# Kernel tuning notes

Measured on AMD Instinct MI355X. Metric: run time of the kernel, lower is better.

## Reference

```python
import jax, jax.numpy as jnp
import numpy as np

B, T, D, V, L = 128, 1024, 512, 128, 128
BLANK = V - 1          # keras ctc_batch_cost uses num_classes-1 as blank
EPS = 1e-7             # tf.keras.backend.epsilon()
NEG = jnp.float32(-1e30)


def setup_inputs() -> dict:
    key = jax.random.key(0)
    k1, k2, k3, k4 = jax.random.split(key, 4)
    x = jax.random.normal(k1, (B, T, D), jnp.float32)
    W = jax.random.normal(k2, (D, V), jnp.float32) / np.sqrt(D)
    b = jnp.zeros((V,), jnp.float32)
    targets = jax.random.randint(k3, (B, L), 0, V - 1, dtype=jnp.int32)   # labels in [0, V-2]
    targets_length = jax.random.randint(k4, (B,), 16, L + 1, dtype=jnp.int32)  # >=1
    return {"x": x, "W": W, "b": b, "targets": targets, "targets_length": targets_length}


def _ctc_neg_log_lik(log_probs, targets, targets_length):
    # log_probs: [B,T,V]; targets: [B,L]; returns per-example -log p(targets | probs)
    Bb, Tt, Vv = log_probs.shape
    Ll = targets.shape[1]
    S = 2 * Ll + 1
    # extended label sequence: blank, l1, blank, l2, ..., blank   [B,S]
    ext = jnp.full((Bb, S), BLANK, dtype=targets.dtype)
    ext = ext.at[:, 1::2].set(targets)
    # allow skip transition s-2 -> s when ext[s] != blank and ext[s] != ext[s-2]
    ext2 = jnp.concatenate([jnp.full((Bb, 2), -1, ext.dtype), ext[:, :-2]], axis=1)
    allow2 = (ext != BLANK) & (ext != ext2)                       # [B,S]

    def emit(logp_t):  # logp_t [B,V] -> [B,S]
        return jnp.take_along_axis(logp_t, ext, axis=1)

    # t = 0: only s=0 (blank) and s=1 (first label) reachable
    e0 = emit(log_probs[:, 0])
    alpha0 = jnp.where(jnp.arange(S)[None, :] < 2, e0, NEG)       # [B,S]

    def step(alpha, logp_t):
        a1 = jnp.concatenate([jnp.full((Bb, 1), NEG), alpha[:, :-1]], axis=1)
        a2 = jnp.concatenate([jnp.full((Bb, 2), NEG), alpha[:, :-2]], axis=1)
        m = jnp.logaddexp(alpha, a1)
        m = jnp.where(allow2, jnp.logaddexp(m, a2), m)
        return m + emit(logp_t), None

    alpha_T, _ = jax.lax.scan(step, alpha0, jnp.swapaxes(log_probs, 0, 1)[1:])
    # final states: s = 2*len (trailing blank) and s = 2*len - 1 (last label)
    last = 2 * targets_length                                     # [B]
    aN = jnp.take_along_axis(alpha_T, last[:, None], axis=1)[:, 0]
    aN1 = jnp.take_along_axis(alpha_T, (last - 1)[:, None], axis=1)[:, 0]
    return -jnp.logaddexp(aN, aN1)                                # [B]


def reference(x, W, b, targets, targets_length):
    # Dense -> Softmax (module outputs probabilities) -> ctc_batch_cost: log(p + eps) -> CTC DP -> sum
    probs = jax.nn.softmax(jnp.einsum("btd,dv->btv", x, W) + b, axis=-1)
    log_probs = jnp.log(probs + EPS)
    loss = _ctc_neg_log_lik(log_probs, targets, targets_length)
    return jnp.sum(loss)
```

## Files before the change

kernel.cpp:

```cpp
#include <hip/hip_runtime.h>

#define Bb 128
#define Tt 1024
#define Dd 512
#define Vv 128
#define Ll 128
#define EPSF 1e-7f
#define PADK 72
#define NEGF -1e30f

typedef float f4 __attribute__((ext_vector_type(4)));
typedef short s8 __attribute__((ext_vector_type(8)));
typedef float f32x4 __attribute__((ext_vector_type(4)));

__device__ inline unsigned int f2bf(float f) {
    unsigned int u = __float_as_uint(f);
    return (u + 0x7fffu + ((u >> 16) & 1u)) >> 16;
}

__device__ inline float lae2(float x, float y) {
    float m = fmaxf(x, y);
    float d = fminf(x, y) - m;
    return m + __logf(1.f + __expf(d));
}

__device__ inline float dpp_shr1(float v) {
    return __int_as_float(__builtin_amdgcn_update_dpp(
        0, __float_as_int(v), 0x138, 0xf, 0xf, false));
}
__device__ inline int dpp_shr1_i(int v) {
    return __builtin_amdgcn_update_dpp(0, v, 0x138, 0xf, 0xf, false);
}

__global__ void wt_kernel(const float* __restrict__ W, unsigned short* __restrict__ Wt) {
    int idx = blockIdx.x * 256 + threadIdx.x;
    int v = idx >> 9, k = idx & 511;
    Wt[idx] = (unsigned short)f2bf(W[k * Vv + v]);
}

__global__ __launch_bounds__(256) void gemm_softmax(
    const float* __restrict__ x, const unsigned short* __restrict__ Wt,
    const float* __restrict__ bias, float* __restrict__ LP)
{
    __shared__ float lds[128 * 128];
    __shared__ __align__(16) float invs[128];
    unsigned short* Al = (unsigned short*)lds;
    unsigned short* Bl = Al + 128 * PADK;

    const int tid = threadIdx.x;
    const int wave = tid >> 6, lane = tid & 63;
    const int lm = lane & 15, lq = lane >> 4;
    const int wm = (wave >> 1) << 6, wn = (wave & 1) << 6;
    const long row0 = (long)blockIdx.x << 7;

    f32x4 acc[4][4];
    #pragma unroll
    for (int i = 0; i < 4; i++)
        #pragma unroll
        for (int j = 0; j < 4; j++)
            acc[i][j] = (f32x4){0.f, 0.f, 0.f, 0.f};

    for (int k0 = 0; k0 < Dd; k0 += 64) {
        __syncthreads();
        #pragma unroll
        for (int i = 0; i < 8; i++) {
            int idx = tid + (i << 8);
            int r = idx >> 4, c4 = idx & 15;
            f4 v = *(const f4*)(x + (row0 + r) * Dd + k0 + (c4 << 2));
            unsigned long long q =
                (unsigned long long)(f2bf(v.x) | (f2bf(v.y) << 16)) |
                ((unsigned long long)(f2bf(v.z) | (f2bf(v.w) << 16)) << 32);
            *(unsigned long long*)(Al + r * PADK + (c4 << 2)) = q;
        }
        #pragma unroll
        for (int i = 0; i < 4; i++) {
            int idx = tid + (i << 8);
            int vr = idx >> 3, c = idx & 7;
            f4 w = *(const f4*)(Wt + vr * 512 + k0 + (c << 3));
            *(f4*)(Bl + vr * PADK + (c << 3)) = w;
        }
        __syncthreads();
        #pragma unroll
        for (int kk = 0; kk < 64; kk += 32) {
            s8 af[4], bfr[4];
            #pragma unroll
            for (int mi = 0; mi < 4; mi++)
                af[mi] = *(const s8*)(Al + (wm + (mi << 4) + lm) * PADK + kk + (lq << 3));
            #pragma unroll
            for (int ni = 0; ni < 4; ni++)
                bfr[ni] = *(const s8*)(Bl + (wn + (ni << 4) + lm) * PADK + kk + (lq << 3));
            #pragma unroll
            for (int mi = 0; mi < 4; mi++)
                #pragma unroll
                for (int ni = 0; ni < 4; ni++)
                    acc[mi][ni] = __builtin_amdgcn_mfma_f32_16x16x32_bf16(
                        af[mi], bfr[ni], acc[mi][ni], 0, 0, 0);
        }
    }
    __syncthreads();
    #pragma unroll
    for (int mi = 0; mi < 4; mi++) {
        #pragma unroll
        for (int ni = 0; ni < 4; ni++) {
            int col = wn + (ni << 4) + lm;
            float bv = bias[col];
            #pragma unroll
            for (int r = 0; r < 4; r++) {
                int row = wm + (mi << 4) + (lq << 2) + r;
                int word = (row << 7) + ((((col >> 2) ^ ((row >> 2) & 7)) & 31) << 2) + (col & 3);
                lds[word] = acc[mi][ni][r] + bv;
            }
        }
    }
    __syncthreads();
    if (tid < 128) {
        int row = tid;
        float m = -1e30f;
        #pragma unroll
        for (int cc = 0; cc < 32; cc++) {
            int word = (row << 7) + (((cc + row) & 31) << 2);
            f4 v = *(const f4*)(lds + word);
            m = fmaxf(m, fmaxf(fmaxf(v.x, v.y), fmaxf(v.z, v.w)));
        }
        float s = 0.f;
        #pragma unroll
        for (int cc = 0; cc < 32; cc++) {
            int word = (row << 7) + (((cc + row) & 31) << 2);
            f4 v = *(f4*)(lds + word);
            v.x = __expf(v.x - m); v.y = __expf(v.y - m);
            v.z = __expf(v.z - m); v.w = __expf(v.w - m);
            s += v.x + v.y + v.z + v.w;
            *(f4*)(lds + word) = v;
        }
        invs[row] = 1.f / s;
    }
    __syncthreads();
    {
        const int l = tid & 31, g = tid >> 5;
        const int bidx = blockIdx.x >> 3;
        const int tbase = (blockIdx.x & 7) << 7;
        const f4 iv = *(const f4*)(invs + (l << 2));
        #pragma unroll
        for (int jj = 0; jj < 16; jj++) {
            const int v = (g << 4) + jj;
            const int swz = ((v >> 2) ^ (l & 7)) << 2;
            const int r0 = v & 3;
            f4 o;
            #pragma unroll
            for (int r = 0; r < 4; r++) {
                int t = (l << 2) + r;
                o[r] = fmaf(lds[(t << 7) + swz + r0], iv[r], EPSF);
            }
            *(f4*)(LP + ((long)bidx * Vv + v) * Tt + tbase + (l << 2)) = o;
        }
    }
}

__global__ __launch_bounds__(64) void ctc_kernel(
    const float* __restrict__ PT, const int* __restrict__ targets,
    const int* __restrict__ tlen, float* __restrict__ out)
{
    const int b = blockIdx.x;
    const int lane = threadIdx.x;
    const float* baseP = PT + (long)b * Vv * Tt;

    const int tgt0 = targets[(b << 7) + (lane << 1)];
    const int tgt1 = targets[(b << 7) + (lane << 1) + 1];
    int tp = __shfl_up(tgt1, 1);
    if (lane == 0) tp = -1;
    const bool mA = (tgt0 != tp);
    const bool mB = (tgt1 != tgt0);
    const float mBf = mB ? 1.f : 0.f;

    const float* pB = baseP + 127 * Tt;
    const float* p0 = baseP + (long)tgt0 * Tt;
    const float* p1 = baseP + (long)tgt1 * Tt;

    float u0 = (lane == 0) ? pB[0] : 0.f;
    float u1 = (lane == 0) ? p0[0] : 0.f;
    float u2 = 0.f, u3 = 0.f, u4 = 0.f;
    int anc = 0;
    float fprev = 1.f;
    float fprevA = mA ? 1.f : 0.f;

    f4 Xb[4], Xs[4], Xt[4], Yb[4], Ys[4], Yt[4], Zb[4], Zs[4], Zt[4];

#define LOADW(BUF, W) do {                                                  \
    int tn_ = ((W) < 63 ? (W) : 63) << 4;                                   \
    _Pragma("unroll")                                                       \
    for (int q = 0; q < 4; q++) {                                           \
        BUF##b[q] = *(const f4*)(pB + tn_ + (q << 2));                      \
        BUF##s[q] = *(const f4*)(p0 + tn_ + (q << 2));                      \
        BUF##t[q] = *(const f4*)(p1 + tn_ + (q << 2));                      \
    } } while (0)

#define DOSTEP(BUF, i) do {                                                 \
    float lb = BUF##b[(i) >> 2][(i) & 3];                                   \
    float l0 = BUF##s[(i) >> 2][(i) & 3];                                   \
    float l1 = BUF##t[(i) >> 2][(i) & 3];                                   \
    float s_ = dpp_shr1(u3);                                \
    float t01 = u0 + u1;                                                    \
    float n0 = fmaf(s_, fprev,  u0) * lb;                                   \
    float n1 = fmaf(s_, fprevA, t01) * l0;                                  \
    float n2 = (u1 + u2) * lb;                                              \
    float n3 = fmaf(u1, mBf, u2 + u3) * l1;                                 \
    float n4 = (u3 + u4) * lb;                                              \
    u0 = n0; u1 = n1; u2 = n2; u3 = n3; u4 = n4; } while (0)

#define RESCALE(ADOPT) do {                                                 \
    float umax = fmaxf(fmaxf(fmaxf(u0, u1), fmaxf(u2, u3)), u4);            \
    int e = (int)((__float_as_uint(umax) >> 23) & 0xffu) - 126;             \
    float sc = __uint_as_float((unsigned)(127 - e) << 23);        \
    u0 *= sc; u1 *= sc; u2 *= sc; u3 *= sc; u4 *= sc;       \
    if (ADOPT) {                                                            \
        bool live = umax > 0.f;                                             \
        anc = live ? (anc + e) : anc;                                       \
        _Pragma("unroll")                                                   \
        for (int r_ = 0; r_ < 3; r_++) {                                    \
            int cp_ = dpp_shr1_i(anc);                                      \
            anc = live ? anc : cp_;                                         \
        }                                                                   \
    } else {                                                                \
        anc += e;                                                           \
    }                                                                       \
    int cp = dpp_shr1_i(anc);                                               \
    int d_ = cp - anc;                                                      \
    d_ = d_ > 96 ? 96 : d_;                     \
    fprev = (d_ < -126) ? 0.f                                               \
           : __uint_as_float((unsigned)((d_ + 127) << 23));                 \
    fprevA = mA ? fprev : 0.f; } while (0)

#define WINDOW(CUR, N2, W, ADOPT, ISTART) do {                              \
    LOADW(N2, (W) + 2);                                                     \
    _Pragma("unroll")                                                       \
    for (int i = ISTART; i < 16; i++) {                                     \
        DOSTEP(CUR, i);                                                     \
        if ((i & 3) == 3) RESCALE(ADOPT);                                   \
    } } while (0)

    LOADW(X, 0);
    LOADW(Y, 1);
    WINDOW(X, Z, 0, true, 1);
    for (int g = 0; g < 5; g++) {
        int w = 1 + 3 * g;
        WINDOW(Y, X, w,     true, 0);
        WINDOW(Z, Y, w + 1, true, 0);
        WINDOW(X, Z, w + 2, true, 0);
    }
    for (int g = 0; g < 16; g++) {
        int w = 16 + 3 * g;
        WINDOW(Y, X, w,     false, 0);
        WINDOW(Z, Y, w + 1, false, 0);
        WINDOW(X, Z, w + 2, false, 0);
    }

    __shared__ float af[257];
    const float LN2 = 0.69314718056f;
    float fa = (float)anc;
    af[(lane << 2) + 0] = u0 > 0.f ? (fa + log2f(u0)) * LN2 : NEGF;
    af[(lane << 2) + 1] = u1 > 0.f ? (fa + log2f(u1)) * LN2 : NEGF;
    af[(lane << 2) + 2] = u2 > 0.f ? (fa + log2f(u2)) * LN2 : NEGF;
    af[(lane << 2) + 3] = u3 > 0.f ? (fa + log2f(u3)) * LN2 : NEGF;
    if (lane == 63) af[256] = u4 > 0.f ? (fa + log2f(u4)) * LN2 : NEGF;
    __syncthreads();
    if (lane == 0) {
        int len = tlen[b];
        float loss = -lae2(af[2 * len], af[2 * len - 1]);
        atomicAdd(out, loss);
    }
}

extern "C" void kernel_launch(void* const* d_in, const int* in_sizes, int n_in,
                              void* d_out, int out_size, void* d_ws, size_t ws_size,
                              hipStream_t stream) {
    const float* x       = (const float*)d_in[0];
    const float* W       = (const float*)d_in[1];
    const float* bias    = (const float*)d_in[2];
    const int*   targets = (const int*)d_in[3];
    const int*   tl      = (const int*)d_in[4];
    float* out = (float*)d_out;

    float* LP = (float*)d_ws;
    unsigned short* Wt = (unsigned short*)((char*)d_ws + (size_t)Bb * Tt * Vv * 4);

    (void)hipMemsetAsync(out, 0, sizeof(float), stream);
    wt_kernel<<<256, 256, 0, stream>>>(W, Wt);
    gemm_softmax<<<1024, 256, 0, stream>>>(x, Wt, bias, LP);
    ctc_kernel<<<Bb, 64, 0, stream>>>(LP, targets, tl, out);
}
```

Before: 434.1 us.

## Double-buffer GEMM LDS tiles with register prefetch and split softmax rows

The GEMM K-loop now prefetches the next x/W tile into registers while MFMAs run on the current LDS buffer, using two ping-pong LDS buffers so only one barrier is needed per tile. The fp32-to-bf16 conversion uses the hardware v_cvt_pk_bf16_f32 instruction instead of manual integer rounding. Softmax row reductions are split across all 256 threads (two per row, combined with shuffles) instead of 128. The aim is to hide global load latency and shorten the epilogue, at the cost of more LDS (72KB) and more registers, which may lower occupancy.

```diff
diff --git a/kernel.cpp b/kernel.cpp
--- a/kernel.cpp
+++ b/kernel.cpp
@@ -42,10 +42,13 @@
     const float* __restrict__ x, const unsigned short* __restrict__ Wt,
     const float* __restrict__ bias, float* __restrict__ LP)
 {
-    __shared__ float lds[128 * 128];
+    __shared__ __align__(16) char smem[73728];
     __shared__ __align__(16) float invs[128];
-    unsigned short* Al = (unsigned short*)lds;
-    unsigned short* Bl = Al + 128 * PADK;
+    unsigned short* Al0 = (unsigned short*)smem;
+    unsigned short* Al1 = (unsigned short*)(smem + 18432);
+    unsigned short* Bl0 = (unsigned short*)(smem + 36864);
+    unsigned short* Bl1 = (unsigned short*)(smem + 55296);
+    float* lds = (float*)smem;
 
     const int tid = threadIdx.x;
     const int wave = tid >> 6, lane = tid & 63;
@@ -60,41 +63,78 @@
         for (int j = 0; j < 4; j++)
             acc[i][j] = (f32x4){0.f, 0.f, 0.f, 0.f};
 
-    for (int k0 = 0; k0 < Dd; k0 += 64) {
+    f4 ra[8], rb[4];
+
+#define STAGE_REGS(K0) do {                                                 \
+    int kb_ = (K0) << 6;                                                    \
+    _Pragma("unroll")                                                       \
+    for (int i = 0; i < 8; i++) {                                           \
+        int idx = tid + (i << 8);                                           \
+        int r = idx >> 4, c4 = idx & 15;                                    \
+        ra[i] = *(const f4*)(x + (row0 + r) * Dd + kb_ + (c4 << 2));        \
+    }                                                                       \
+    _Pragma("unroll")                                                       \
+    for (int i = 0; i < 4; i++) {                                           \
+        int idx = tid + (i << 8);                                           \
+        int vr = idx >> 3, c = idx & 7;                                     \
+        rb[i] = *(const f4*)(Wt + vr * 512 + kb_ + (c << 3));               \
+    } } while (0)
+
+#define WRITE_LDS(AL, BL) do {                                              \
+    _Pragma("unroll")                                                       \
+    for (int i = 0; i < 8; i++) {                                           \
+        int idx = tid + (i << 8);                                           \
+        int r = idx >> 4, c4 = idx & 15;                                    \
+        unsigned int lo_, hi_;                                              \
+        asm("v_cvt_pk_bf16_f32 %0, %1, %2" : "=v"(lo_)                      \
+            : "v"(ra[i].x), "v"(ra[i].y));                                  \
+        asm("v_cvt_pk_bf16_f32 %0, %1, %2" : "=v"(hi_)                      \
+            : "v"(ra[i].z), "v"(ra[i].w));                                  \
+        unsigned long long q_ = (unsigned long long)lo_                     \
+                              | ((unsigned long long)hi_ << 32);            \
+        *(unsigned long long*)((AL) + r * PADK + (c4 << 2)) = q_;           \
+    }                                                                       \
+    _Pragma("unroll")                                                       \
+    for (int i = 0; i < 4; i++) {                                           \
+        int idx = tid + (i << 8);                                           \
+        int vr = idx >> 3, c = idx & 7;                                     \
+        *(f4*)((BL) + vr * PADK + (c << 3)) = rb[i];                        \
+    } } while (0)
+
+#define MFMA_TILE(AL, BL) do {                                              \
+    _Pragma("unroll")                                                       \
+    for (int kk = 0; kk < 64; kk += 32) {                                   \
+        s8 afr[4], bfr[4];                                                  \
+        _Pragma("unroll")                                                   \
+        for (int mi = 0; mi < 4; mi++)                                      \
+            afr[mi] = *(const s8*)((AL) + (wm + (mi << 4) + lm) * PADK      \
+                                    + kk + (lq << 3));                      \
+        _Pragma("unroll")                                                   \
+        for (int ni = 0; ni < 4; ni++)                                      \
+            bfr[ni] = *(const s8*)((BL) + (wn + (ni << 4) + lm) * PADK      \
+                                    + kk + (lq << 3));                      \
+        _Pragma("unroll")                                                   \
+        for (int mi = 0; mi < 4; mi++)                                      \
+            _Pragma("unroll")                                               \
+            for (int ni = 0; ni < 4; ni++)                                  \
+                acc[mi][ni] = __builtin_amdgcn_mfma_f32_16x16x32_bf16(      \
+                    afr[mi], bfr[ni], acc[mi][ni], 0, 0, 0);                \
+    } } while (0)
+
+    STAGE_REGS(0);
+    WRITE_LDS(Al0, Bl0);
+    __syncthreads();
+    #pragma unroll
+    for (int s = 0; s < 4; s++) {
+        STAGE_REGS(2 * s + 1);
+        MFMA_TILE(Al0, Bl0);
+        WRITE_LDS(Al1, Bl1);
         __syncthreads();
-        #pragma unroll
-        for (int i = 0; i < 8; i++) {
-            int idx = tid + (i << 8);
-            int r = idx >> 4, c4 = idx & 15;
-            f4 v = *(const f4*)(x + (row0 + r) * Dd + k0 + (c4 << 2));
-            unsigned long long q =
-                (unsigned long long)(f2bf(v.x) | (f2bf(v.y) << 16)) |
-                ((unsigned long long)(f2bf(v.z) | (f2bf(v.w) << 16)) << 32);
-            *(unsigned long long*)(Al + r * PADK + (c4 << 2)) = q;
-        }
-        #pragma unroll
-        for (int i = 0; i < 4; i++) {
-            int idx = tid + (i << 8);
-            int vr = idx >> 3, c = idx & 7;
-            f4 w = *(const f4*)(Wt + vr * 512 + k0 + (c << 3));
-            *(f4*)(Bl + vr * PADK + (c << 3)) = w;
-        }
-        __syncthreads();
-        #pragma unroll
-        for (int kk = 0; kk < 64; kk += 32) {
-            s8 af[4], bfr[4];
-            #pragma unroll
-            for (int mi = 0; mi < 4; mi++)
-                af[mi] = *(const s8*)(Al + (wm + (mi << 4) + lm) * PADK + kk + (lq << 3));
-            #pragma unroll
-            for (int ni = 0; ni < 4; ni++)
-                bfr[ni] = *(const s8*)(Bl + (wn + (ni << 4) + lm) * PADK + kk + (lq << 3));
-            #pragma unroll
-            for (int mi = 0; mi < 4; mi++)
-                #pragma unroll
-                for (int ni = 0; ni < 4; ni++)
-                    acc[mi][ni] = __builtin_amdgcn_mfma_f32_16x16x32_bf16(
-                        af[mi], bfr[ni], acc[mi][ni], 0, 0, 0);
+        if (s < 3) STAGE_REGS(2 * s + 2);
+        MFMA_TILE(Al1, Bl1);
+        if (s < 3) {
+            WRITE_LDS(Al0, Bl0);
+            __syncthreads();
         }
     }
     __syncthreads();
@@ -113,26 +153,28 @@
         }
     }
     __syncthreads();
-    if (tid < 128) {
-        int row = tid;
+    {
+        const int row = tid >> 1, h = tid & 1;
         float m = -1e30f;
         #pragma unroll
-        for (int cc = 0; cc < 32; cc++) {
-            int word = (row << 7) + (((cc + row) & 31) << 2);
+        for (int cc = 0; cc < 16; cc++) {
+            int word = (row << 7) + (((cc + (h << 4) + row) & 31) << 2);
             f4 v = *(const f4*)(lds + word);
             m = fmaxf(m, fmaxf(fmaxf(v.x, v.y), fmaxf(v.z, v.w)));
         }
+        m = fmaxf(m, __shfl_xor(m, 1));
         float s = 0.f;
         #pragma unroll
-        for (int cc = 0; cc < 32; cc++) {
-            int word = (row << 7) + (((cc + row) & 31) << 2);
+        for (int cc = 0; cc < 16; cc++) {
+            int word = (row << 7) + (((cc + (h << 4) + row) & 31) << 2);
             f4 v = *(f4*)(lds + word);
             v.x = __expf(v.x - m); v.y = __expf(v.y - m);
             v.z = __expf(v.z - m); v.w = __expf(v.w - m);
             s += v.x + v.y + v.z + v.w;
             *(f4*)(lds + word) = v;
         }
-        invs[row] = 1.f / s;
+        s += __shfl_xor(s, 1);
+        if (h == 0) invs[row] = 1.f / s;
     }
     __syncthreads();
     {
@@ -154,6 +196,9 @@
             *(f4*)(LP + ((long)bidx * Vv + v) * Tt + tbase + (l << 2)) = o;
         }
     }
+#undef STAGE_REGS
+#undef WRITE_LDS
+#undef MFMA_TILE
 }
 
 __global__ __launch_bounds__(64) void ctc_kernel(
```

New measurement: 442.2 us. Within noise of the previous version (+1.9%).
